# Performance work log

Hardware: AMD Instinct MI355X
Metric: run time of the kernel (lower is better)

Reference implementation:

```python
import jax, jax.numpy as jnp
import numpy as np

N = 200000
E = 3200000
NHID = 128
NUM_GRAPHS = 512


def setup_inputs() -> dict:
    key = jax.random.key(0)
    k_x, k_ei, k_b, k_n, k_w1, k_w2, k_bl = jax.random.split(key, 7)
    x = jax.random.normal(k_x, (N, NHID), dtype=jnp.float32)
    edge_index = jax.random.randint(k_ei, (2, E), 0, N, dtype=jnp.int32)
    batch = jnp.sort(jax.random.randint(k_b, (N,), 0, NUM_GRAPHS, dtype=jnp.int32))
    noise = jax.random.normal(k_n, (N, NHID), dtype=jnp.float32)
    # Generator params (xavier-ish init)
    h = NHID // 2
    W1 = jax.random.normal(k_w1, (NHID, h), dtype=jnp.float32) * np.float32(1.0 / np.sqrt(NHID))
    b1 = jnp.zeros((h,), dtype=jnp.float32)
    W2 = jax.random.normal(k_w2, (h, NHID), dtype=jnp.float32) * np.float32(1.0 / np.sqrt(h))
    b2 = jnp.zeros((NHID,), dtype=jnp.float32)
    return {"x": x, "edge_index": edge_index, "batch": batch, "noise": noise,
            "W1": W1, "b1": b1, "W2": W2, "b2": b2}


def scatter_mean(src_feats, dst_idx, num_nodes):
    # sum messages per destination node, then divide by in-degree (clamped to 1)
    summed = jax.ops.segment_sum(src_feats, dst_idx, num_segments=num_nodes)
    counts = jax.ops.segment_sum(jnp.ones((src_feats.shape[0],), src_feats.dtype),
                                 dst_idx, num_segments=num_nodes)
    return summed / jnp.maximum(counts, 1.0)[:, None]


def reference(x, edge_index, batch, noise, W1, b1, W2, b2):
    src, dst = edge_index[0], edge_index[1]
    # NeighborPropagate: mean aggregation of x_j = x[src] at dst
    x_neighbor = scatter_mean(x[src], dst, x.shape[0])  # [N, nhid]
    g = x_neighbor + noise
    # Generator MLP: relu(fc2(relu(fc1(g))))
    h = jax.nn.relu(g @ W1 + b1)
    x_gen = jax.nn.relu(h @ W2 + b2)
    return x_gen
```

## Files before the change

kernel.cpp:

```cpp
#include <hip/hip_runtime.h>

#define NHID 128
#define HDIM 64
#define EPB 8192
#define MAXBKT 1024
#define CAP 6144

typedef __attribute__((ext_vector_type(8))) short bf16x8;
typedef __attribute__((ext_vector_type(4))) float f32x4;

__device__ __forceinline__ unsigned short f2bf_rn(float f) {
    union { float f; unsigned u; } c; c.f = f;
    unsigned r = c.u + 0x7fffu + ((c.u >> 16) & 1u);
    return (unsigned short)(r >> 16);
}
__device__ __forceinline__ float bf_lo(unsigned d) {
    union { unsigned u; float f; } c; c.u = d << 16; return c.f;
}
__device__ __forceinline__ float bf_hi(unsigned d) {
    union { unsigned u; float f; } c; c.u = d & 0xFFFF0000u; return c.f;
}

__global__ __launch_bounds__(256) void prep_bf16(const float* __restrict__ x,
                                                 unsigned short* __restrict__ xh,
                                                 long long total8) {
    long long t = (long long)blockIdx.x * blockDim.x + threadIdx.x;
    if (t >= total8) return;
    const float4 a = *(const float4*)(x + t * 8);
    const float4 b = *(const float4*)(x + t * 8 + 4);
    ushort4 p, q;
    p.x = f2bf_rn(a.x); p.y = f2bf_rn(a.y); p.z = f2bf_rn(a.z); p.w = f2bf_rn(a.w);
    q.x = f2bf_rn(b.x); q.y = f2bf_rn(b.y); q.z = f2bf_rn(b.z); q.w = f2bf_rn(b.w);
    *(ushort4*)(xh + t * 8) = p;
    *(ushort4*)(xh + t * 8 + 4) = q;
}

__global__ __launch_bounds__(256) void bucket_scatter(const int* __restrict__ src,
                                                      const int* __restrict__ dst,
                                                      int* __restrict__ bucket_cursor,
                                                      unsigned int* __restrict__ bpack,
                                                      int E, int NBKT) {
    __shared__ int h[MAXBKT];
    int t = threadIdx.x;
    long long base = (long long)blockIdx.x * EPB;
    for (int i = t; i < NBKT; i += 256) h[i] = 0;
    __syncthreads();
    for (int p = 0; p < EPB / 256; ++p) {
        long long e = base + p * 256 + t;
        if (e < E) atomicAdd(&h[((unsigned)dst[e]) >> 8], 1);
    }
    __syncthreads();
    for (int i = t; i < NBKT; i += 256) {
        int c = h[i];
        h[i] = c ? (i * CAP + atomicAdd(&bucket_cursor[i], c)) : 0;
    }
    __syncthreads();
    for (int p = 0; p < EPB / 256; ++p) {
        long long e = base + p * 256 + t;
        if (e < E) {
            int d = dst[e];
            int s = src[e];
            int b = ((unsigned)d) >> 8;
            int pos = atomicAdd(&h[b], 1);
            if (pos < (b + 1) * CAP)
                bpack[pos] = (((unsigned)d & 255u) << 24) | (unsigned)s;
        }
    }
}

__global__ __launch_bounds__(256) void bucket_build(unsigned int* __restrict__ bpack,
                                                    const int* __restrict__ bucket_cursor,
                                                    int* __restrict__ cnt,
                                                    int* __restrict__ rowptr,
                                                    int N) {
    __shared__ unsigned ebuf[CAP];
    __shared__ int lc[256];
    __shared__ int sc[256];
    int b = blockIdx.x, t = threadIdx.x;
    int beg = b * CAP;
    int m = bucket_cursor[b]; if (m > CAP) m = CAP;
    lc[t] = 0;
    __syncthreads();
    for (int i = t; i < m; i += 256) {
        unsigned v = bpack[beg + i];
        ebuf[i] = v;
        atomicAdd(&lc[v >> 24], 1);
    }
    __syncthreads();
    int myc = lc[t];
    sc[t] = myc; __syncthreads();
    for (int off = 1; off < 256; off <<= 1) {
        int v = (t >= off) ? sc[t - off] : 0;
        __syncthreads();
        sc[t] += v;
        __syncthreads();
    }
    int excl = sc[t] - myc;
    int node = b * 256 + t;
    if (node < N) { cnt[node] = myc; rowptr[node] = beg + excl; }
    lc[t] = excl;
    __syncthreads();
    for (int i = t; i < m; i += 256) {
        unsigned v = ebuf[i];
        int pos = atomicAdd(&lc[v >> 24], 1);
        bpack[beg + pos] = v & 0xFFFFFFu;
    }
}

__global__ __launch_bounds__(256) void gather_fuse(
    const unsigned short* __restrict__ xh, const unsigned int* __restrict__ perm,
    const int* __restrict__ rowptr, const int* __restrict__ cnt,
    const float* __restrict__ noise, unsigned short* __restrict__ g, int N)
{
    long long t = (long long)blockIdx.x * blockDim.x + threadIdx.x;
    int n = (int)(t >> 4);
    int c = (int)(t & 15);
    if (n >= N) return;
    int beg = rowptr[n];
    int deg = cnt[n];
    float a0 = 0.f, a1 = 0.f, a2 = 0.f, a3 = 0.f, a4 = 0.f, a5 = 0.f, a6 = 0.f, a7 = 0.f;
    const unsigned short* xb = xh + c * 8;
    int i = 0;
    for (; i + 3 < deg; i += 4) {
        unsigned s0 = perm[beg + i];
        unsigned s1 = perm[beg + i + 1];
        unsigned s2 = perm[beg + i + 2];
        unsigned s3 = perm[beg + i + 3];
        uint4 u0 = *(const uint4*)(xb + (long long)s0 * NHID);
        uint4 u1 = *(const uint4*)(xb + (long long)s1 * NHID);
        uint4 u2 = *(const uint4*)(xb + (long long)s2 * NHID);
        uint4 u3 = *(const uint4*)(xb + (long long)s3 * NHID);
        a0 += (bf_lo(u0.x) + bf_lo(u1.x)) + (bf_lo(u2.x) + bf_lo(u3.x));
        a1 += (bf_hi(u0.x) + bf_hi(u1.x)) + (bf_hi(u2.x) + bf_hi(u3.x));
        a2 += (bf_lo(u0.y) + bf_lo(u1.y)) + (bf_lo(u2.y) + bf_lo(u3.y));
        a3 += (bf_hi(u0.y) + bf_hi(u1.y)) + (bf_hi(u2.y) + bf_hi(u3.y));
        a4 += (bf_lo(u0.z) + bf_lo(u1.z)) + (bf_lo(u2.z) + bf_lo(u3.z));
        a5 += (bf_hi(u0.z) + bf_hi(u1.z)) + (bf_hi(u2.z) + bf_hi(u3.z));
        a6 += (bf_lo(u0.w) + bf_lo(u1.w)) + (bf_lo(u2.w) + bf_lo(u3.w));
        a7 += (bf_hi(u0.w) + bf_hi(u1.w)) + (bf_hi(u2.w) + bf_hi(u3.w));
    }
    for (; i < deg; ++i) {
        unsigned s0 = perm[beg + i];
        uint4 u = *(const uint4*)(xb + (long long)s0 * NHID);
        a0 += bf_lo(u.x); a1 += bf_hi(u.x);
        a2 += bf_lo(u.y); a3 += bf_hi(u.y);
        a4 += bf_lo(u.z); a5 += bf_hi(u.z);
        a6 += bf_lo(u.w); a7 += bf_hi(u.w);
    }
    float inv = 1.0f / fmaxf((float)deg, 1.0f);
    const float* nr = noise + (long long)n * NHID + c * 8;
    float4 n0 = *(const float4*)nr;
    float4 n1 = *(const float4*)(nr + 4);
    ushort4 p, q;
    p.x = f2bf_rn(fmaf(a0, inv, n0.x));
    p.y = f2bf_rn(fmaf(a1, inv, n0.y));
    p.z = f2bf_rn(fmaf(a2, inv, n0.z));
    p.w = f2bf_rn(fmaf(a3, inv, n0.w));
    q.x = f2bf_rn(fmaf(a4, inv, n1.x));
    q.y = f2bf_rn(fmaf(a5, inv, n1.y));
    q.z = f2bf_rn(fmaf(a6, inv, n1.z));
    q.w = f2bf_rn(fmaf(a7, inv, n1.w));
    unsigned short* go = g + (long long)n * 256 + c * 8;
    *(ushort4*)go = p;
    *(ushort4*)(go + 4) = q;
}

__global__ __launch_bounds__(256) void mlp_mfma(
    float* out,
    const float* __restrict__ W1, const float* __restrict__ b1,
    const float* __restrict__ W2, const float* __restrict__ b2,
    int N)
{
    __shared__ __align__(16) unsigned short w1t[64 * 136];
    __shared__ __align__(16) unsigned short w2t[128 * 72];
    __shared__ __align__(16) unsigned short ht[4][16 * 72];
    __shared__ float b1s[HDIM];
    __shared__ float b2s[NHID];

    int t = threadIdx.x;
    int wave = t >> 6;
    int lane = t & 63;
    int m = lane & 15;
    int quad = lane >> 4;

    #pragma unroll 4
    for (int p = 0; p < 32; ++p) {
        int idx = p * 256 + t;
        int k = idx >> 6, n = idx & 63;
        w1t[n * 136 + k] = f2bf_rn(W1[idx]);
    }
    #pragma unroll 4
    for (int p = 0; p < 32; ++p) {
        int idx = p * 256 + t;
        int k = idx >> 7, n = idx & 127;
        w2t[n * 72 + k] = f2bf_rn(W2[idx]);
    }
    if (t < HDIM) b1s[t] = b1[t];
    else if (t < HDIM + NHID) b2s[t - HDIM] = b2[t - HDIM];
    __syncthreads();

    int node = blockIdx.x * 64 + wave * 16 + m;
    int nodec = node < N ? node : N - 1;

    const unsigned short* grow = (const unsigned short*)out + (long long)nodec * 256;
    bf16x8 afrag[4];
    #pragma unroll
    for (int kc = 0; kc < 4; ++kc)
        afrag[kc] = *(const bf16x8*)(grow + kc * 32 + quad * 8);

    unsigned short* hw = &ht[wave][0];
    #pragma unroll
    for (int nt = 0; nt < 4; ++nt) {
        f32x4 acc = {0.f, 0.f, 0.f, 0.f};
        #pragma unroll
        for (int kc = 0; kc < 4; ++kc) {
            bf16x8 bfrag = *(const bf16x8*)&w1t[(nt * 16 + m) * 136 + kc * 32 + quad * 8];
            acc = __builtin_amdgcn_mfma_f32_16x16x32_bf16(afrag[kc], bfrag, acc, 0, 0, 0);
        }
        float bb = b1s[nt * 16 + m];
        #pragma unroll
        for (int r = 0; r < 4; ++r) {
            hw[(quad * 4 + r) * 72 + nt * 16 + m] = f2bf_rn(fmaxf(acc[r] + bb, 0.0f));
        }
    }

    bf16x8 a2[2];
    #pragma unroll
    for (int kc = 0; kc < 2; ++kc)
        a2[kc] = *(const bf16x8*)&hw[m * 72 + kc * 32 + quad * 8];

    float* obase = out + ((long long)blockIdx.x * 64 + wave * 16) * NHID;
    #pragma unroll
    for (int nt = 0; nt < 8; ++nt) {
        f32x4 acc = {0.f, 0.f, 0.f, 0.f};
        #pragma unroll
        for (int kc = 0; kc < 2; ++kc) {
            bf16x8 bfrag = *(const bf16x8*)&w2t[(nt * 16 + m) * 72 + kc * 32 + quad * 8];
            acc = __builtin_amdgcn_mfma_f32_16x16x32_bf16(a2[kc], bfrag, acc, 0, 0, 0);
        }
        float bb = b2s[nt * 16 + m];
        #pragma unroll
        for (int r = 0; r < 4; ++r) {
            int orow = blockIdx.x * 64 + wave * 16 + quad * 4 + r;
            if (orow < N)
                obase[(quad * 4 + r) * NHID + nt * 16 + m] = fmaxf(acc[r] + bb, 0.0f);
        }
    }
}

extern "C" void kernel_launch(void* const* d_in, const int* in_sizes, int n_in,
                              void* d_out, int out_size, void* d_ws, size_t ws_size,
                              hipStream_t stream) {
    const float* x     = (const float*)d_in[0];
    const int*   ei    = (const int*)d_in[1];
    const float* noise = (const float*)d_in[3];
    const float* W1    = (const float*)d_in[4];
    const float* b1    = (const float*)d_in[5];
    const float* W2    = (const float*)d_in[6];
    const float* b2    = (const float*)d_in[7];
    float* out = (float*)d_out;

    const int N = in_sizes[2];
    const int E = in_sizes[1] / 2;
    const int* src = ei;
    const int* dst = ei + E;
    const int NBKT = (N + 255) >> 8;

    int* bucket_cursor = (int*)d_ws;
    int* cnt           = bucket_cursor + MAXBKT;
    int* rowptr        = cnt + N;
    unsigned int* bpack = (unsigned int*)(rowptr + N);
    unsigned short* xh  = (unsigned short*)(bpack + (size_t)NBKT * CAP);

    hipMemsetAsync(bucket_cursor, 0, (size_t)MAXBKT * sizeof(int), stream);

    {
        long long total8 = (long long)N * NHID / 8;
        prep_bf16<<<(int)((total8 + 255) / 256), 256, 0, stream>>>(x, xh, total8);
    }
    {
        const int EB = (int)(((long long)E + EPB - 1) / EPB);
        bucket_scatter<<<EB, 256, 0, stream>>>(src, dst, bucket_cursor, bpack, E, NBKT);
    }
    bucket_build<<<NBKT, 256, 0, stream>>>(bpack, bucket_cursor, cnt, rowptr, N);
    {
        long long total = (long long)N * 16;
        gather_fuse<<<(int)((total + 255) / 256), 256, 0, stream>>>(
            xh, bpack, rowptr, cnt, noise, (unsigned short*)out, N);
    }
    mlp_mfma<<<(N + 63) / 64, 256, 0, stream>>>(out, W1, b1, W2, b2, N);
}
```

Baseline: 490.9 us.

## Fuse bucket sort and neighbor gather into one per-bucket kernel using LDS

Merges the per-bucket counting sort with the mean-gather so each 512-thread block sorts its bucket's edges into shared memory and then aggregates its 256 destination nodes directly. This removes the write-back of sorted edges and the rowptr/cnt arrays to global memory and one kernel launch. The trade-off is that the gather now runs with only NBKT (~782) blocks of 512 threads, far fewer than the previous node-parallel grid, which may reduce the latency hiding available for the random x-row loads.

```diff
diff --git a/kernel.cpp b/kernel.cpp
--- a/kernel.cpp
+++ b/kernel.cpp
@@ -68,101 +68,117 @@
     }
 }
 
-__global__ __launch_bounds__(256) void bucket_build(unsigned int* __restrict__ bpack,
-                                                    const int* __restrict__ bucket_cursor,
-                                                    int* __restrict__ cnt,
-                                                    int* __restrict__ rowptr,
-                                                    int N) {
-    __shared__ unsigned ebuf[CAP];
-    __shared__ int lc[256];
-    __shared__ int sc[256];
+__global__ __launch_bounds__(512) void bucket_sort_gather(
+    const unsigned short* __restrict__ xh,
+    const unsigned int* __restrict__ bpack,
+    const int* __restrict__ bucket_cursor,
+    const float* __restrict__ noise,
+    unsigned short* __restrict__ g, int N)
+{
+    __shared__ unsigned sbuf[CAP];
+    __shared__ int hist_[256];
+    __shared__ int rp[256];
+    __shared__ int cnt_[256];
     int b = blockIdx.x, t = threadIdx.x;
     int beg = b * CAP;
     int m = bucket_cursor[b]; if (m > CAP) m = CAP;
-    lc[t] = 0;
-    __syncthreads();
-    for (int i = t; i < m; i += 256) {
-        unsigned v = bpack[beg + i];
-        ebuf[i] = v;
-        atomicAdd(&lc[v >> 24], 1);
-    }
-    __syncthreads();
-    int myc = lc[t];
-    sc[t] = myc; __syncthreads();
+
+    if (t < 256) hist_[t] = 0;
+    __syncthreads();
+
+    unsigned ent[CAP / 512];
+    #pragma unroll
+    for (int j = 0; j < CAP / 512; ++j) {
+        int i = t + j * 512;
+        ent[j] = 0u;
+        if (i < m) {
+            unsigned v = bpack[beg + i];
+            ent[j] = v;
+            atomicAdd(&hist_[v >> 24], 1);
+        }
+    }
+    __syncthreads();
+
+    if (t < 256) cnt_[t] = hist_[t];
+    __syncthreads();
     for (int off = 1; off < 256; off <<= 1) {
-        int v = (t >= off) ? sc[t - off] : 0;
+        int v = 0;
+        if (t < 256 && t >= off) v = hist_[t - off];
         __syncthreads();
-        sc[t] += v;
+        if (t < 256) hist_[t] += v;
         __syncthreads();
     }
-    int excl = sc[t] - myc;
-    int node = b * 256 + t;
-    if (node < N) { cnt[node] = myc; rowptr[node] = beg + excl; }
-    lc[t] = excl;
-    __syncthreads();
-    for (int i = t; i < m; i += 256) {
-        unsigned v = ebuf[i];
-        int pos = atomicAdd(&lc[v >> 24], 1);
-        bpack[beg + pos] = v & 0xFFFFFFu;
-    }
-}
-
-__global__ __launch_bounds__(256) void gather_fuse(
-    const unsigned short* __restrict__ xh, const unsigned int* __restrict__ perm,
-    const int* __restrict__ rowptr, const int* __restrict__ cnt,
-    const float* __restrict__ noise, unsigned short* __restrict__ g, int N)
-{
-    long long t = (long long)blockIdx.x * blockDim.x + threadIdx.x;
-    int n = (int)(t >> 4);
-    int c = (int)(t & 15);
-    if (n >= N) return;
-    int beg = rowptr[n];
-    int deg = cnt[n];
-    float a0 = 0.f, a1 = 0.f, a2 = 0.f, a3 = 0.f, a4 = 0.f, a5 = 0.f, a6 = 0.f, a7 = 0.f;
+    if (t < 256) {
+        rp[t] = hist_[t] - cnt_[t];
+        hist_[t] = rp[t];
+    }
+    __syncthreads();
+
+    #pragma unroll
+    for (int j = 0; j < CAP / 512; ++j) {
+        int i = t + j * 512;
+        if (i < m) {
+            unsigned v = ent[j];
+            int pos = atomicAdd(&hist_[v >> 24], 1);
+            sbuf[pos] = v & 0xFFFFFFu;
+        }
+    }
+    __syncthreads();
+
+    int c   = t & 15;
+    int grp = t >> 4;
     const unsigned short* xb = xh + c * 8;
-    int i = 0;
-    for (; i + 3 < deg; i += 4) {
-        unsigned s0 = perm[beg + i];
-        unsigned s1 = perm[beg + i + 1];
-        unsigned s2 = perm[beg + i + 2];
-        unsigned s3 = perm[beg + i + 3];
-        uint4 u0 = *(const uint4*)(xb + (long long)s0 * NHID);
-        uint4 u1 = *(const uint4*)(xb + (long long)s1 * NHID);
-        uint4 u2 = *(const uint4*)(xb + (long long)s2 * NHID);
-        uint4 u3 = *(const uint4*)(xb + (long long)s3 * NHID);
-        a0 += (bf_lo(u0.x) + bf_lo(u1.x)) + (bf_lo(u2.x) + bf_lo(u3.x));
-        a1 += (bf_hi(u0.x) + bf_hi(u1.x)) + (bf_hi(u2.x) + bf_hi(u3.x));
-        a2 += (bf_lo(u0.y) + bf_lo(u1.y)) + (bf_lo(u2.y) + bf_lo(u3.y));
-        a3 += (bf_hi(u0.y) + bf_hi(u1.y)) + (bf_hi(u2.y) + bf_hi(u3.y));
-        a4 += (bf_lo(u0.z) + bf_lo(u1.z)) + (bf_lo(u2.z) + bf_lo(u3.z));
-        a5 += (bf_hi(u0.z) + bf_hi(u1.z)) + (bf_hi(u2.z) + bf_hi(u3.z));
-        a6 += (bf_lo(u0.w) + bf_lo(u1.w)) + (bf_lo(u2.w) + bf_lo(u3.w));
-        a7 += (bf_hi(u0.w) + bf_hi(u1.w)) + (bf_hi(u2.w) + bf_hi(u3.w));
-    }
-    for (; i < deg; ++i) {
-        unsigned s0 = perm[beg + i];
-        uint4 u = *(const uint4*)(xb + (long long)s0 * NHID);
-        a0 += bf_lo(u.x); a1 += bf_hi(u.x);
-        a2 += bf_lo(u.y); a3 += bf_hi(u.y);
-        a4 += bf_lo(u.z); a5 += bf_hi(u.z);
-        a6 += bf_lo(u.w); a7 += bf_hi(u.w);
-    }
-    float inv = 1.0f / fmaxf((float)deg, 1.0f);
-    const float* nr = noise + (long long)n * NHID + c * 8;
-    float4 n0 = *(const float4*)nr;
-    float4 n1 = *(const float4*)(nr + 4);
-    ushort4 p, q;
-    p.x = f2bf_rn(fmaf(a0, inv, n0.x));
-    p.y = f2bf_rn(fmaf(a1, inv, n0.y));
-    p.z = f2bf_rn(fmaf(a2, inv, n0.z));
-    p.w = f2bf_rn(fmaf(a3, inv, n0.w));
-    q.x = f2bf_rn(fmaf(a4, inv, n1.x));
-    q.y = f2bf_rn(fmaf(a5, inv, n1.y));
-    q.z = f2bf_rn(fmaf(a6, inv, n1.z));
-    q.w = f2bf_rn(fmaf(a7, inv, n1.w));
-    unsigned short* go = g + (long long)n * 256 + c * 8;
-    *(ushort4*)go = p;
-    *(ushort4*)(go + 4) = q;
+    for (int dn = grp; dn < 256; dn += 32) {
+        int node = b * 256 + dn;
+        if (node >= N) continue;
+        int deg  = cnt_[dn];
+        int rbeg = rp[dn];
+        float a0 = 0.f, a1 = 0.f, a2 = 0.f, a3 = 0.f,
+              a4 = 0.f, a5 = 0.f, a6 = 0.f, a7 = 0.f;
+        int i = 0;
+        for (; i + 3 < deg; i += 4) {
+            unsigned s0 = sbuf[rbeg + i];
+            unsigned s1 = sbuf[rbeg + i + 1];
+            unsigned s2 = sbuf[rbeg + i + 2];
+            unsigned s3 = sbuf[rbeg + i + 3];
+            uint4 u0 = *(const uint4*)(xb + (long long)s0 * NHID);
+            uint4 u1 = *(const uint4*)(xb + (long long)s1 * NHID);
+            uint4 u2 = *(const uint4*)(xb + (long long)s2 * NHID);
+            uint4 u3 = *(const uint4*)(xb + (long long)s3 * NHID);
+            a0 += (bf_lo(u0.x) + bf_lo(u1.x)) + (bf_lo(u2.x) + bf_lo(u3.x));
+            a1 += (bf_hi(u0.x) + bf_hi(u1.x)) + (bf_hi(u2.x) + bf_hi(u3.x));
+            a2 += (bf_lo(u0.y) + bf_lo(u1.y)) + (bf_lo(u2.y) + bf_lo(u3.y));
+            a3 += (bf_hi(u0.y) + bf_hi(u1.y)) + (bf_hi(u2.y) + bf_hi(u3.y));
+            a4 += (bf_lo(u0.z) + bf_lo(u1.z)) + (bf_lo(u2.z) + bf_lo(u3.z));
+            a5 += (bf_hi(u0.z) + bf_hi(u1.z)) + (bf_hi(u2.z) + bf_hi(u3.z));
+            a6 += (bf_lo(u0.w) + bf_lo(u1.w)) + (bf_lo(u2.w) + bf_lo(u3.w));
+            a7 += (bf_hi(u0.w) + bf_hi(u1.w)) + (bf_hi(u2.w) + bf_hi(u3.w));
+        }
+        for (; i < deg; ++i) {
+            unsigned s0 = sbuf[rbeg + i];
+            uint4 u = *(const uint4*)(xb + (long long)s0 * NHID);
+            a0 += bf_lo(u.x); a1 += bf_hi(u.x);
+            a2 += bf_lo(u.y); a3 += bf_hi(u.y);
+            a4 += bf_lo(u.z); a5 += bf_hi(u.z);
+            a6 += bf_lo(u.w); a7 += bf_hi(u.w);
+        }
+        float inv = 1.0f / fmaxf((float)deg, 1.0f);
+        const float* nr = noise + (long long)node * NHID + c * 8;
+        float4 n0 = *(const float4*)nr;
+        float4 n1 = *(const float4*)(nr + 4);
+        ushort4 p, q;
+        p.x = f2bf_rn(fmaf(a0, inv, n0.x));
+        p.y = f2bf_rn(fmaf(a1, inv, n0.y));
+        p.z = f2bf_rn(fmaf(a2, inv, n0.z));
+        p.w = f2bf_rn(fmaf(a3, inv, n0.w));
+        q.x = f2bf_rn(fmaf(a4, inv, n1.x));
+        q.y = f2bf_rn(fmaf(a5, inv, n1.y));
+        q.z = f2bf_rn(fmaf(a6, inv, n1.z));
+        q.w = f2bf_rn(fmaf(a7, inv, n1.w));
+        unsigned short* go = g + (long long)node * 256 + c * 8;
+        *(ushort4*)go = p;
+        *(ushort4*)(go + 4) = q;
+    }
 }
 
 __global__ __launch_bounds__(256) void mlp_mfma(
@@ -267,9 +283,7 @@
     const int NBKT = (N + 255) >> 8;
 
     int* bucket_cursor = (int*)d_ws;
-    int* cnt           = bucket_cursor + MAXBKT;
-    int* rowptr        = cnt + N;
-    unsigned int* bpack = (unsigned int*)(rowptr + N);
+    unsigned int* bpack = (unsigned int*)(bucket_cursor + MAXBKT);
     unsigned short* xh  = (unsigned short*)(bpack + (size_t)NBKT * CAP);
 
     hipMemsetAsync(bucket_cursor, 0, (size_t)MAXBKT * sizeof(int), stream);
@@ -282,11 +296,7 @@
         const int EB = (int)(((long long)E + EPB - 1) / EPB);
         bucket_scatter<<<EB, 256, 0, stream>>>(src, dst, bucket_cursor, bpack, E, NBKT);
     }
-    bucket_build<<<NBKT, 256, 0, stream>>>(bpack, bucket_cursor, cnt, rowptr, N);
-    {
-        long long total = (long long)N * 16;
-        gather_fuse<<<(int)((total + 255) / 256), 256, 0, stream>>>(
-            xh, bpack, rowptr, cnt, noise, (unsigned short*)out, N);
-    }
+    bucket_sort_gather<<<NBKT, 512, 0, stream>>>(
+        xh, bpack, bucket_cursor, noise, (unsigned short*)out, N);
     mlp_mfma<<<(N + 63) / 64, 256, 0, stream>>>(out, W1, b1, W2, b2, N);
 }
```

After: 497.3 us. Within noise of the previous version (+1.3%).

## Stage bucketed edges in shared memory for coalesced global writes

Applied to the files above, without the earlier changes.

The bucket scatter kernel now first sorts each block's edges by bucket inside a shared-memory buffer, using a local prefix scan over bucket counts. It then writes them out contiguously per bucket, finding each element's bucket by binary search. This replaces random scattered global stores with mostly contiguous runs, at the cost of 32KB+ of extra LDS per block, a scan, and a binary search per edge, which may reduce occupancy.

```diff
diff --git a/kernel.cpp b/kernel.cpp
--- a/kernel.cpp
+++ b/kernel.cpp
@@ -41,29 +41,72 @@
                                                       unsigned int* __restrict__ bpack,
                                                       int E, int NBKT) {
     __shared__ int h[MAXBKT];
+    __shared__ int lofs[MAXBKT];
+    __shared__ int lcur[MAXBKT];
+    __shared__ unsigned sbuf[EPB];
     int t = threadIdx.x;
     long long base = (long long)blockIdx.x * EPB;
-    for (int i = t; i < NBKT; i += 256) h[i] = 0;
-    __syncthreads();
+    int rem = (int)(E - base);
+    int nev = rem < EPB ? rem : EPB;
+
+    for (int i = t; i < MAXBKT; i += 256) h[i] = 0;
+    __syncthreads();
+
     for (int p = 0; p < EPB / 256; ++p) {
-        long long e = base + p * 256 + t;
-        if (e < E) atomicAdd(&h[((unsigned)dst[e]) >> 8], 1);
-    }
-    __syncthreads();
-    for (int i = t; i < NBKT; i += 256) {
+        int e = p * 256 + t;
+        if (e < nev) atomicAdd(&h[((unsigned)dst[base + e]) >> 8], 1);
+    }
+    __syncthreads();
+
+    #pragma unroll
+    for (int j = 0; j < 4; ++j) lofs[t + j * 256] = h[t + j * 256];
+    __syncthreads();
+    for (int off = 1; off < MAXBKT; off <<= 1) {
+        int v0, v1, v2, v3;
+        {
+            int i0 = t, i1 = t + 256, i2 = t + 512, i3 = t + 768;
+            v0 = lofs[i0] + (i0 >= off ? lofs[i0 - off] : 0);
+            v1 = lofs[i1] + (i1 >= off ? lofs[i1 - off] : 0);
+            v2 = lofs[i2] + (i2 >= off ? lofs[i2 - off] : 0);
+            v3 = lofs[i3] + (i3 >= off ? lofs[i3 - off] : 0);
+        }
+        __syncthreads();
+        lofs[t] = v0; lofs[t + 256] = v1; lofs[t + 512] = v2; lofs[t + 768] = v3;
+        __syncthreads();
+    }
+
+    for (int i = t; i < MAXBKT; i += 256) {
         int c = h[i];
+        lcur[i] = lofs[i] - c;
         h[i] = c ? (i * CAP + atomicAdd(&bucket_cursor[i], c)) : 0;
     }
     __syncthreads();
+
     for (int p = 0; p < EPB / 256; ++p) {
-        long long e = base + p * 256 + t;
-        if (e < E) {
-            int d = dst[e];
-            int s = src[e];
+        int e = p * 256 + t;
+        if (e < nev) {
+            int d = dst[base + e];
+            int s = src[base + e];
             int b = ((unsigned)d) >> 8;
-            int pos = atomicAdd(&h[b], 1);
-            if (pos < (b + 1) * CAP)
-                bpack[pos] = (((unsigned)d & 255u) << 24) | (unsigned)s;
+            int pos = atomicAdd(&lcur[b], 1);
+            sbuf[pos] = (((unsigned)d & 255u) << 24) | (unsigned)s;
+        }
+    }
+    __syncthreads();
+
+    for (int p = 0; p < EPB / 256; ++p) {
+        int j = p * 256 + t;
+        if (j < nev) {
+            int lo = 0, hi = NBKT - 1;
+            while (lo < hi) {
+                int mid = (lo + hi) >> 1;
+                if (lofs[mid] > j) hi = mid; else lo = mid + 1;
+            }
+            int b = lo;
+            int prev = b ? lofs[b - 1] : 0;
+            int gpos = h[b] + (j - prev);
+            if (gpos < (b + 1) * CAP)
+                bpack[gpos] = sbuf[j];
         }
     }
 }
```

New measurement: 480.6 us. 1.02x faster.
